# Kernel tuning notes

Hardware: AMD Instinct MI355X
Metric: run time of the kernel (lower is better)

Reference implementation:

```python
import jax, jax.numpy as jnp
import numpy as np

B, L, V, H = 2, 2048, 1024, 16
HD = V // H  # head size 64
EPS = 1e-3   # keras LayerNormalization default


def setup_inputs() -> dict:
    key = jax.random.key(0)
    ks = jax.random.split(key, 10)
    scale = 1.0 / np.sqrt(V)
    return {
        "query": jax.random.normal(ks[0], (B, L, V), jnp.float32),
        "key_t": jax.random.normal(ks[1], (B, L, V), jnp.float32),
        "value": jax.random.normal(ks[2], (B, L, V), jnp.float32),
        "Wq": jax.random.normal(ks[3], (H, V, HD), jnp.float32) * scale,
        "Wk": jax.random.normal(ks[4], (H, V, HD), jnp.float32) * scale,
        "Wv": jax.random.normal(ks[5], (H, V, HD), jnp.float32) * scale,
        "gamma": jnp.ones((V,), jnp.float32),
        "beta": jnp.zeros((V,), jnp.float32),
        "query_mask": jax.random.randint(ks[6], (B, L), 0, 2, jnp.int32),
        "value_mask": jax.random.randint(ks[7], (B, L), 0, 2, jnp.int32),
    }


def reference(query, key_t, value, Wq, Wk, Wv, gamma, beta, query_mask, value_mask):
    qm = query_mask.astype(jnp.float32)  # (B,L)
    vm = value_mask.astype(jnp.float32)  # (B,L)

    # per-head no-bias Dense projections, batched over heads
    Q = jnp.einsum('blv,hvd->bhld', query, Wq)
    K = jnp.einsum('blv,hvd->bhld', key_t, Wk)
    Vh = jnp.einsum('blv,hvd->bhld', value, Wv)

    scores = jnp.einsum('bhld,bhmd->bhlm', Q, K) / jnp.sqrt(jnp.float32(HD))
    attn = jax.nn.softmax(scores, axis=-1)

    # post-softmax multiplicative masking (faithful to original)
    tri = jnp.tril(jnp.ones((L, L), jnp.float32))  # (L,L) causal
    attn = attn * tri[None, None, :, :]
    attn = attn * qm[:, None, :, None] * vm[:, None, None, :]

    heads = jnp.einsum('bhlm,bhmd->bhld', attn, Vh)
    x = heads.transpose(0, 2, 1, 3).reshape(B, L, V)  # concat heads

    # dropout is identity at inference
    y = x + query
    mu = jnp.mean(y, axis=-1, keepdims=True)
    var = jnp.mean((y - mu) ** 2, axis=-1, keepdims=True)
    return gamma * (y - mu) * jax.lax.rsqrt(var + EPS) + beta
```

## Files before the change

kernel.cpp:

```cpp
#include <hip/hip_runtime.h>
#include <math.h>

constexpr int NB = 2;
constexpr int SL = 2048;
constexpr int NV = 1024;
constexpr int NH = 16;
constexpr int DH = 64;
constexpr int NT = SL / 64;
constexpr float LN_EPS = 1e-3f;

typedef __bf16 bf16_t;
typedef __bf16 v8bf __attribute__((ext_vector_type(8)));
typedef float  v4f  __attribute__((ext_vector_type(4)));

__device__ __forceinline__ v8bf cvt8(float4 a, float4 b) {
  v8bf v;
  v[0] = (bf16_t)a.x; v[1] = (bf16_t)a.y; v[2] = (bf16_t)a.z; v[3] = (bf16_t)a.w;
  v[4] = (bf16_t)b.x; v[5] = (bf16_t)b.y; v[6] = (bf16_t)b.z; v[7] = (bf16_t)b.w;
  return v;
}
__device__ __forceinline__ unsigned pack_bf16(float a, float b) {
  unsigned short ua = __builtin_bit_cast(unsigned short, (bf16_t)a);
  unsigned short ub = __builtin_bit_cast(unsigned short, (bf16_t)b);
  return (unsigned)ua | ((unsigned)ub << 16);
}
__device__ __forceinline__ void async_cp16(const void* g, void* l) {
  __builtin_amdgcn_global_load_lds(
      (const __attribute__((address_space(1))) unsigned int*)g,
      (__attribute__((address_space(3))) unsigned int*)l, 16, 0, 0);
}

__global__ __launch_bounds__(256)
void wcvt(const float* __restrict__ Wq, const float* __restrict__ Wk,
          const float* __restrict__ Wv, bf16_t* __restrict__ Wt) {
  __shared__ float ls[64][65];
  const int z = blockIdx.z;
  const float* W = z == 0 ? Wq : (z == 1 ? Wk : Wv);
  const float sc = z == 0 ? 0.125f * 1.44269504f : 1.0f;
  const int h = blockIdx.y, v0 = blockIdx.x * 64;
  const int t = threadIdx.x;
  const int rr = t >> 4, c4 = t & 15;
  const float* src = W + ((size_t)h * NV + v0) * DH;
#pragma unroll
  for (int it = 0; it < 4; ++it) {
    float4 f = *(const float4*)(src + (size_t)(rr + it * 16) * DH + c4 * 4);
    ls[rr + it * 16][c4 * 4 + 0] = f.x;
    ls[rr + it * 16][c4 * 4 + 1] = f.y;
    ls[rr + it * 16][c4 * 4 + 2] = f.z;
    ls[rr + it * 16][c4 * 4 + 3] = f.w;
  }
  __syncthreads();
  const int dd = t >> 2, vq = t & 3;
  bf16_t tmp[16];
#pragma unroll
  for (int i = 0; i < 16; ++i) tmp[i] = (bf16_t)(ls[vq * 16 + i][dd] * sc);
  bf16_t* dst = Wt + ((size_t)z * NV + h * 64 + dd) * NV + v0 + vq * 16;
  *(v8bf*)dst = *(v8bf*)&tmp[0];
  *(v8bf*)(dst + 8) = *(v8bf*)&tmp[8];
}

__global__ __launch_bounds__(256, 3)
void proj_mfma(const float* __restrict__ A0, const float* __restrict__ A1,
               const float* __restrict__ A2, const bf16_t* __restrict__ Wtb,
               const int* __restrict__ vmask,
               bf16_t* __restrict__ O0, bf16_t* __restrict__ O1,
               bf16_t* __restrict__ O2) {
  __shared__ __align__(16) float  As[2][128 * 32];
  __shared__ __align__(16) bf16_t Wsh[2][128 * 32];

  const int z = blockIdx.z;
  const float*  A   = z == 0 ? A0 : (z == 1 ? A1 : A2);
  bf16_t*       out = z == 0 ? O0 : (z == 1 ? O1 : O2);
  const bf16_t* W   = Wtb + (size_t)z * NV * NV;

  const int t = threadIdx.x, w = t >> 6, lane = t & 63;
  const int g = lane >> 4, lx = lane & 15;
  const int m0 = blockIdx.x * 128, n0 = blockIdx.y * 128;
  const int rbase = (w >> 1) * 64, cbase = (w & 1) * 64;

  auto stageA = [&](int k0, int buf) {
#pragma unroll
    for (int s = 0; s < 4; ++s) {
      const int r = w * 32 + s * 8 + (lane >> 3);
      const int c = (lane & 7) ^ (r & 7);
      async_cp16(A + (size_t)(m0 + r) * NV + k0 + c * 4,
                 (char*)As[buf] + (w * 32 + s * 8) * 128);
    }
  };
  auto stageW = [&](int k0, int buf) {
#pragma unroll
    for (int s = 0; s < 2; ++s) {
      const int r = w * 32 + s * 16 + (lane >> 2);
      const int c = (lane & 3) ^ (r & 3);
      async_cp16(W + (size_t)(n0 + r) * NV + k0 + c * 8,
                 (char*)Wsh[buf] + (w * 32 + s * 16) * 64);
    }
  };

  v4f acc[4][4] = {};
  stageA(0, 0);
  stageW(0, 0);

  for (int k0 = 0; k0 < NV; k0 += 32) {
    const int buf = (k0 >> 5) & 1;
    __syncthreads();
    if (k0 + 32 < NV) { stageA(k0 + 32, buf ^ 1); stageW(k0 + 32, buf ^ 1); }
    v8bf af[4], wf[4];
#pragma unroll
    for (int rt = 0; rt < 4; ++rt) {
      const int row = rbase + rt * 16 + lx;
      const int sw = row & 7;
      float4 f0 = *(const float4*)((const char*)As[buf] + row * 128 + ((2 * g)     ^ sw) * 16);
      float4 f1 = *(const float4*)((const char*)As[buf] + row * 128 + ((2 * g + 1) ^ sw) * 16);
      af[rt] = cvt8(f0, f1);
    }
#pragma unroll
    for (int ct = 0; ct < 4; ++ct) {
      const int row = cbase + ct * 16 + lx;
      wf[ct] = *(const v8bf*)((const char*)Wsh[buf] + row * 64 + (g ^ (row & 3)) * 16);
    }
#pragma unroll
    for (int rt = 0; rt < 4; ++rt)
#pragma unroll
      for (int ct = 0; ct < 4; ++ct)
        acc[rt][ct] = __builtin_amdgcn_mfma_f32_16x16x32_bf16(
            af[rt], wf[ct], acc[rt][ct], 0, 0, 0);
  }

  if (z < 2) {
#pragma unroll
    for (int rt = 0; rt < 4; ++rt) {
#pragma unroll
      for (int reg = 0; reg < 4; ++reg) {
        const int row = m0 + rbase + rt * 16 + g * 4 + reg;
        const int b = row >> 11, l = row & (SL - 1);
#pragma unroll
        for (int ct = 0; ct < 4; ++ct) {
          const int n = n0 + cbase + ct * 16 + lx;
          const int h = n >> 6, d = n & 63;
          out[((size_t)(b * NH + h) * SL + l) * DH + d] = (bf16_t)acc[rt][ct][reg];
        }
      }
    }
  } else {
#pragma unroll
    for (int rt = 0; rt < 4; ++rt) {
      const int row = m0 + rbase + rt * 16 + g * 4;
      const int b = row >> 11, l = row & (SL - 1);
      float vm0 = (float)vmask[b * SL + l + 0];
      float vm1 = (float)vmask[b * SL + l + 1];
      float vm2 = (float)vmask[b * SL + l + 2];
      float vm3 = (float)vmask[b * SL + l + 3];
#pragma unroll
      for (int ct = 0; ct < 4; ++ct) {
        const int n = n0 + cbase + ct * 16 + lx;
        const int h = n >> 6, d = n & 63;
        uint2 u = {pack_bf16(acc[rt][ct][0] * vm0, acc[rt][ct][1] * vm1),
                   pack_bf16(acc[rt][ct][2] * vm2, acc[rt][ct][3] * vm3)};
        *(uint2*)&out[((size_t)(b * NH + h) * DH + d) * SL + l] = u;
      }
    }
  }
}

__global__ __launch_bounds__(256, 3)
void attn_mfma(const bf16_t* __restrict__ Qg, const bf16_t* __restrict__ Kg,
               const bf16_t* __restrict__ Vtg_all, const int* __restrict__ qmask,
               float* __restrict__ Xout) {
  struct LoopBufs { bf16_t kbuf[2][64 * 64]; bf16_t vbuf[2][64 * 64]; };
  union __align__(16) SU { LoopBufs lp; float Obuf[2][64][36]; };
  __shared__ SU su;
  __shared__ bf16_t Ps[64][72];
  __shared__ float sums[2][64];

  const int id = blockIdx.x;
  const int bh = (id & 7) | ((id >> 8) << 3);
  const int qb = 31 - ((id >> 3) & 31);
  const int t = threadIdx.x, w = t >> 6, lane = t & 63;
  const int g = lane >> 4, lx = lane & 15;
  const int mh = w >> 1, qh = w & 1;
  const int b = bh >> 4, h = bh & 15;
  const int l0 = qb * 64;

  const bf16_t* Kb  = Kg + (size_t)bh * SL * DH;
  const bf16_t* Vtg = Vtg_all + (size_t)bh * DH * SL;

  v8bf qf[2][2];
#pragma unroll
  for (int qt = 0; qt < 2; ++qt)
#pragma unroll
    for (int ks = 0; ks < 2; ++ks)
      qf[qt][ks] = *(const v8bf*)&Qg[((size_t)bh * SL + l0 + qh * 32 + qt * 16 + lx) * DH +
                                     ks * 32 + g * 8];

  v4f O[2][4] = {};
  float suml[2] = {0.f, 0.f};

  auto stageK = [&](int mb, int buf) {
#pragma unroll
    for (int s = 0; s < 2; ++s) {
      const int r = w * 16 + s * 8 + (lane >> 3);
      const int c = (lane & 7) ^ (r & 7);
      async_cp16(Kb + (size_t)(mb + r) * DH + c * 8,
                 (char*)su.lp.kbuf[buf] + (w * 16 + s * 8) * 128);
    }
  };
  auto stageV = [&](int mb, int buf) {
#pragma unroll
    for (int s = 0; s < 2; ++s) {
      const int r = w * 16 + s * 8 + (lane >> 3);
      const int c = (lane & 7) ^ (r & 7);
      async_cp16(Vtg + (size_t)r * SL + mb + c * 8,
                 (char*)su.lp.vbuf[buf] + (w * 16 + s * 8) * 128);
    }
  };

  stageK(0, 0);
  stageV(0, 0);

  for (int mt = 0; mt <= qb; ++mt) {
    const int m0 = mt * 64, pb = mt & 1;
    __syncthreads();
    if (mt + 1 < NT)  stageK(m0 + 64, pb ^ 1);
    if (mt + 1 <= qb) stageV(m0 + 64, pb ^ 1);

    v4f S[2][2] = {};
#pragma unroll
    for (int ks = 0; ks < 2; ++ks)
#pragma unroll
      for (int mt2 = 0; mt2 < 2; ++mt2) {
        const int row = mh * 32 + mt2 * 16 + lx;
        const int slot = (ks * 4 + g) ^ (row & 7);
        v8bf kf = *(const v8bf*)((const char*)su.lp.kbuf[pb] + row * 128 + slot * 16);
#pragma unroll
        for (int qt = 0; qt < 2; ++qt)
          S[mt2][qt] = __builtin_amdgcn_mfma_f32_16x16x32_bf16(
              kf, qf[qt][ks], S[mt2][qt], 0, 0, 0);
      }

    const bool diag = (mt == qb);
#pragma unroll
    for (int mt2 = 0; mt2 < 2; ++mt2)
#pragma unroll
      for (int qt = 0; qt < 2; ++qt) {
        float e0 = __builtin_amdgcn_exp2f(S[mt2][qt][0]);
        float e1 = __builtin_amdgcn_exp2f(S[mt2][qt][1]);
        float e2 = __builtin_amdgcn_exp2f(S[mt2][qt][2]);
        float e3 = __builtin_amdgcn_exp2f(S[mt2][qt][3]);
        suml[qt] += (e0 + e1) + (e2 + e3);
        if (diag) {
          const int ml = mh * 32 + mt2 * 16 + g * 4;
          const int ql = qh * 32 + qt * 16 + lx;
          e0 = (ml + 0 <= ql) ? e0 : 0.f;
          e1 = (ml + 1 <= ql) ? e1 : 0.f;
          e2 = (ml + 2 <= ql) ? e2 : 0.f;
          e3 = (ml + 3 <= ql) ? e3 : 0.f;
        }
        uint2 u = {pack_bf16(e0, e1), pack_bf16(e2, e3)};
        *(uint2*)&Ps[qh * 32 + qt * 16 + lx][mh * 32 + mt2 * 16 + g * 4] = u;
      }

    v8bf pf[2];
#pragma unroll
    for (int qt = 0; qt < 2; ++qt)
      pf[qt] = *(const v8bf*)&Ps[qh * 32 + qt * 16 + lx][mh * 32 + g * 8];
#pragma unroll
    for (int dt = 0; dt < 4; ++dt) {
      const int row = dt * 16 + lx;
      const int slot = (mh * 4 + g) ^ (row & 7);
      v8bf vf = *(const v8bf*)((const char*)su.lp.vbuf[pb] + row * 128 + slot * 16);
#pragma unroll
      for (int qt = 0; qt < 2; ++qt)
        O[qt][dt] = __builtin_amdgcn_mfma_f32_16x16x32_bf16(
            pf[qt], vf, O[qt][dt], 0, 0, 0);
    }
  }

  for (int mt = qb + 1; mt < NT; ++mt) {
    const int pb = mt & 1;
    __syncthreads();
    if (mt + 1 < NT) stageK(mt * 64 + 64, pb ^ 1);
    v4f S[2][2] = {};
#pragma unroll
    for (int ks = 0; ks < 2; ++ks)
#pragma unroll
      for (int mt2 = 0; mt2 < 2; ++mt2) {
        const int row = mh * 32 + mt2 * 16 + lx;
        const int slot = (ks * 4 + g) ^ (row & 7);
        v8bf kf = *(const v8bf*)((const char*)su.lp.kbuf[pb] + row * 128 + slot * 16);
#pragma unroll
        for (int qt = 0; qt < 2; ++qt)
          S[mt2][qt] = __builtin_amdgcn_mfma_f32_16x16x32_bf16(
              kf, qf[qt][ks], S[mt2][qt], 0, 0, 0);
      }
#pragma unroll
    for (int mt2 = 0; mt2 < 2; ++mt2)
#pragma unroll
      for (int qt = 0; qt < 2; ++qt)
        suml[qt] += (__builtin_amdgcn_exp2f(S[mt2][qt][0]) +
                     __builtin_amdgcn_exp2f(S[mt2][qt][1])) +
                    (__builtin_amdgcn_exp2f(S[mt2][qt][2]) +
                     __builtin_amdgcn_exp2f(S[mt2][qt][3]));
  }

  suml[0] += __shfl_xor(suml[0], 16); suml[0] += __shfl_xor(suml[0], 32);
  suml[1] += __shfl_xor(suml[1], 16); suml[1] += __shfl_xor(suml[1], 32);
  __syncthreads();
  if (g == 0) {
    sums[mh][qh * 32 + lx]      = suml[0];
    sums[mh][qh * 32 + 16 + lx] = suml[1];
  }
  if (mh == 0) {
#pragma unroll
    for (int qt = 0; qt < 2; ++qt)
#pragma unroll
      for (int dt = 0; dt < 4; ++dt)
        *(v4f*)&su.Obuf[qh][dt * 16 + lx][qt * 16 + g * 4] = O[qt][dt];
  }
  __syncthreads();
  if (mh == 1) {
#pragma unroll
    for (int qt = 0; qt < 2; ++qt) {
#pragma unroll
      for (int dt = 0; dt < 4; ++dt)
        O[qt][dt] += *(const v4f*)&su.Obuf[qh][dt * 16 + lx][qt * 16 + g * 4];
#pragma unroll
      for (int reg = 0; reg < 4; ++reg) {
        const int ql = qh * 32 + qt * 16 + g * 4 + reg;
        const int q = l0 + ql;
        const float den = sums[0][ql] + sums[1][ql];
        const float inv = (float)qmask[b * SL + q] / den;
#pragma unroll
        for (int dt = 0; dt < 4; ++dt)
          Xout[((size_t)(b * SL + q)) * NV + h * DH + dt * 16 + lx] =
              O[qt][dt][reg] * inv;
      }
    }
  }
}

__global__ __launch_bounds__(256)
void ln_kernel(const float* __restrict__ X, const float* __restrict__ query,
               const float* __restrict__ gamma, const float* __restrict__ beta,
               float* __restrict__ out) {
  const int row0 = blockIdx.x * 2;
  const int t = threadIdx.x;
  float4 gv = *(const float4*)(gamma + t * 4);
  float4 bv = *(const float4*)(beta + t * 4);
  float y[2][4];
  float s[2], ss[2];
#pragma unroll
  for (int r = 0; r < 2; ++r) {
    float4 xv = *(const float4*)(X + (size_t)(row0 + r) * NV + t * 4);
    float4 qv = *(const float4*)(query + (size_t)(row0 + r) * NV + t * 4);
    y[r][0] = xv.x + qv.x; y[r][1] = xv.y + qv.y;
    y[r][2] = xv.z + qv.z; y[r][3] = xv.w + qv.w;
    s[r]  = (y[r][0] + y[r][1]) + (y[r][2] + y[r][3]);
    ss[r] = (y[r][0]*y[r][0] + y[r][1]*y[r][1]) + (y[r][2]*y[r][2] + y[r][3]*y[r][3]);
  }
#pragma unroll
  for (int off = 1; off < 64; off <<= 1) {
    s[0]  += __shfl_xor(s[0], off);  ss[0] += __shfl_xor(ss[0], off);
    s[1]  += __shfl_xor(s[1], off);  ss[1] += __shfl_xor(ss[1], off);
  }
  __shared__ float wsum[2][2][4];
  const int wid = t >> 6;
  if ((t & 63) == 0) {
    wsum[0][0][wid] = s[0]; wsum[0][1][wid] = ss[0];
    wsum[1][0][wid] = s[1]; wsum[1][1][wid] = ss[1];
  }
  __syncthreads();
#pragma unroll
  for (int r = 0; r < 2; ++r) {
    float sr  = (wsum[r][0][0] + wsum[r][0][1]) + (wsum[r][0][2] + wsum[r][0][3]);
    float ssr = (wsum[r][1][0] + wsum[r][1][1]) + (wsum[r][1][2] + wsum[r][1][3]);
    const float mu   = sr * (1.f / NV);
    const float var  = ssr * (1.f / NV) - mu * mu;
    const float rstd = rsqrtf(var + LN_EPS);
    float4 o;
    o.x = gv.x * (y[r][0] - mu) * rstd + bv.x;
    o.y = gv.y * (y[r][1] - mu) * rstd + bv.y;
    o.z = gv.z * (y[r][2] - mu) * rstd + bv.z;
    o.w = gv.w * (y[r][3] - mu) * rstd + bv.w;
    *(float4*)(out + (size_t)(row0 + r) * NV + t * 4) = o;
  }
}

extern "C" void kernel_launch(void* const* d_in, const int* in_sizes, int n_in,
                              void* d_out, int out_size, void* d_ws, size_t ws_size,
                              hipStream_t stream) {
  const float* query = (const float*)d_in[0];
  const float* key_t = (const float*)d_in[1];
  const float* value = (const float*)d_in[2];
  const float* Wq    = (const float*)d_in[3];
  const float* Wk    = (const float*)d_in[4];
  const float* Wv    = (const float*)d_in[5];
  const float* gamma = (const float*)d_in[6];
  const float* beta  = (const float*)d_in[7];
  const int*   qmask = (const int*)d_in[8];
  const int*   vmask = (const int*)d_in[9];
  float* out = (float*)d_out;

  const size_t per = (size_t)NB * NH * SL * DH;
  bf16_t* Qws = (bf16_t*)d_ws;
  bf16_t* Kws = Qws + per;
  bf16_t* Vws = Kws + per;
  bf16_t* Wtb = Vws + per;

  wcvt<<<dim3(16, 16, 3), 256, 0, stream>>>(Wq, Wk, Wv, Wtb);
  proj_mfma<<<dim3(32, 8, 3), 256, 0, stream>>>(query, key_t, value, Wtb,
                                                vmask, Qws, Kws, Vws);
  attn_mfma<<<1024, 256, 0, stream>>>(Qws, Kws, Vws, qmask, out);
  ln_kernel<<<NB * SL / 2, 256, 0, stream>>>(out, query, gamma, beta, out);
}
```

Measured before the change: 226.8 us.

## Enlarge attention query tile and convert projection A tiles to bf16 in registers

The attention kernel now gives each block 128 query rows, with each wave owning 32 queries across all 64 keys of a tile. This drops the cross-wave O and sum reduction through shared memory and halves the number of K/V tile loads per query. The projection kernel now loads fp32 activations into registers, converts them to bf16, and writes bf16 to padded LDS instead of staging fp32 with async copies, which halves LDS footprint and read traffic. In exchange the grid shrinks to 512 attention blocks, giving less parallelism and worse causal load balance, and the synchronous global loads for A may expose latency.

Measured after the change: 226.8 us. No clear change (-0.0%).

```diff
diff --git a/kernel.cpp b/kernel.cpp
--- a/kernel.cpp
+++ b/kernel.cpp
@@ -6,19 +6,12 @@
 constexpr int NV = 1024;
 constexpr int NH = 16;
 constexpr int DH = 64;
-constexpr int NT = SL / 64;
 constexpr float LN_EPS = 1e-3f;
 
 typedef __bf16 bf16_t;
 typedef __bf16 v8bf __attribute__((ext_vector_type(8)));
 typedef float  v4f  __attribute__((ext_vector_type(4)));
 
-__device__ __forceinline__ v8bf cvt8(float4 a, float4 b) {
-  v8bf v;
-  v[0] = (bf16_t)a.x; v[1] = (bf16_t)a.y; v[2] = (bf16_t)a.z; v[3] = (bf16_t)a.w;
-  v[4] = (bf16_t)b.x; v[5] = (bf16_t)b.y; v[6] = (bf16_t)b.z; v[7] = (bf16_t)b.w;
-  return v;
-}
 __device__ __forceinline__ unsigned pack_bf16(float a, float b) {
   unsigned short ua = __builtin_bit_cast(unsigned short, (bf16_t)a);
   unsigned short ub = __builtin_bit_cast(unsigned short, (bf16_t)b);
@@ -65,27 +58,37 @@
                const int* __restrict__ vmask,
                bf16_t* __restrict__ O0, bf16_t* __restrict__ O1,
                bf16_t* __restrict__ O2) {
-  __shared__ __align__(16) float  As[2][128 * 32];
-  __shared__ __align__(16) bf16_t Wsh[2][128 * 32];
-
-  const int z = blockIdx.z;
+  __shared__ __align__(16) bf16_t Asb[2][128 * 40];
+  __shared__ __align__(16) bf16_t Wsb[2][128 * 32];
+
+  const int id = blockIdx.x;
+  const int z = id >> 8;
+  const int m0 = (id & 31) * 128;
+  const int n0 = ((id >> 5) & 7) * 128;
   const float*  A   = z == 0 ? A0 : (z == 1 ? A1 : A2);
   bf16_t*       out = z == 0 ? O0 : (z == 1 ? O1 : O2);
   const bf16_t* W   = Wtb + (size_t)z * NV * NV;
 
   const int t = threadIdx.x, w = t >> 6, lane = t & 63;
   const int g = lane >> 4, lx = lane & 15;
-  const int m0 = blockIdx.x * 128, n0 = blockIdx.y * 128;
   const int rbase = (w >> 1) * 64, cbase = (w & 1) * 64;
 
-  auto stageA = [&](int k0, int buf) {
-#pragma unroll
-    for (int s = 0; s < 4; ++s) {
-      const int r = w * 32 + s * 8 + (lane >> 3);
-      const int c = (lane & 7) ^ (r & 7);
-      async_cp16(A + (size_t)(m0 + r) * NV + k0 + c * 4,
-                 (char*)As[buf] + (w * 32 + s * 8) * 128);
-    }
+  const int ar_r = t >> 1;
+  const int ar_h = (t & 1) * 16;
+  float4 ar[4];
+  auto gloadA = [&](int k0) {
+#pragma unroll
+    for (int s = 0; s < 4; ++s)
+      ar[s] = *(const float4*)(A + (size_t)(m0 + ar_r) * NV + k0 + ar_h + s * 4);
+  };
+  auto writeA = [&](int buf) {
+    const int c0 = (ar_h >> 3);
+    uint4 u0 = {pack_bf16(ar[0].x, ar[0].y), pack_bf16(ar[0].z, ar[0].w),
+                pack_bf16(ar[1].x, ar[1].y), pack_bf16(ar[1].z, ar[1].w)};
+    uint4 u1 = {pack_bf16(ar[2].x, ar[2].y), pack_bf16(ar[2].z, ar[2].w),
+                pack_bf16(ar[3].x, ar[3].y), pack_bf16(ar[3].z, ar[3].w)};
+    *(uint4*)((char*)Asb[buf] + ar_r * 80 + (c0 + 0) * 16) = u0;
+    *(uint4*)((char*)Asb[buf] + ar_r * 80 + (c0 + 1) * 16) = u1;
   };
   auto stageW = [&](int k0, int buf) {
 #pragma unroll
@@ -93,31 +96,31 @@
       const int r = w * 32 + s * 16 + (lane >> 2);
       const int c = (lane & 3) ^ (r & 3);
       async_cp16(W + (size_t)(n0 + r) * NV + k0 + c * 8,
-                 (char*)Wsh[buf] + (w * 32 + s * 16) * 64);
+                 (char*)Wsb[buf] + (w * 32 + s * 16) * 64);
     }
   };
 
   v4f acc[4][4] = {};
-  stageA(0, 0);
+
+  gloadA(0);
   stageW(0, 0);
-
-  for (int k0 = 0; k0 < NV; k0 += 32) {
-    const int buf = (k0 >> 5) & 1;
-    __syncthreads();
-    if (k0 + 32 < NV) { stageA(k0 + 32, buf ^ 1); stageW(k0 + 32, buf ^ 1); }
+  writeA(0);
+  __syncthreads();
+
+  for (int it = 0; it < 32; ++it) {
+    const int buf = it & 1;
+    if (it < 31) { gloadA((it + 1) * 32); stageW((it + 1) * 32, buf ^ 1); }
     v8bf af[4], wf[4];
 #pragma unroll
     for (int rt = 0; rt < 4; ++rt) {
       const int row = rbase + rt * 16 + lx;
-      const int sw = row & 7;
-      float4 f0 = *(const float4*)((const char*)As[buf] + row * 128 + ((2 * g)     ^ sw) * 16);
-      float4 f1 = *(const float4*)((const char*)As[buf] + row * 128 + ((2 * g + 1) ^ sw) * 16);
-      af[rt] = cvt8(f0, f1);
+      af[rt] = *(const v8bf*)((const char*)Asb[buf] + row * 80 + g * 16);
     }
 #pragma unroll
     for (int ct = 0; ct < 4; ++ct) {
       const int row = cbase + ct * 16 + lx;
-      wf[ct] = *(const v8bf*)((const char*)Wsh[buf] + row * 64 + (g ^ (row & 3)) * 16);
+      wf[ct] = *(const v8bf*)((const char*)Wsb[buf] + row * 64 +
+                              ((g ^ (row & 3)) * 16));
     }
 #pragma unroll
     for (int rt = 0; rt < 4; ++rt)
@@ -125,6 +128,7 @@
       for (int ct = 0; ct < 4; ++ct)
         acc[rt][ct] = __builtin_amdgcn_mfma_f32_16x16x32_bf16(
             af[rt], wf[ct], acc[rt][ct], 0, 0, 0);
+    if (it < 31) { writeA(buf ^ 1); __syncthreads(); }
   }
 
   if (z < 2) {
@@ -167,20 +171,18 @@
 void attn_mfma(const bf16_t* __restrict__ Qg, const bf16_t* __restrict__ Kg,
                const bf16_t* __restrict__ Vtg_all, const int* __restrict__ qmask,
                float* __restrict__ Xout) {
-  struct LoopBufs { bf16_t kbuf[2][64 * 64]; bf16_t vbuf[2][64 * 64]; };
-  union __align__(16) SU { LoopBufs lp; float Obuf[2][64][36]; };
-  __shared__ SU su;
-  __shared__ bf16_t Ps[64][72];
-  __shared__ float sums[2][64];
+  __shared__ __align__(16) bf16_t kbuf[2][64 * 64];
+  __shared__ __align__(16) bf16_t vbuf[2][64 * 64];
+  __shared__ __align__(16) bf16_t Ps[4][32][72];
 
   const int id = blockIdx.x;
-  const int bh = (id & 7) | ((id >> 8) << 3);
-  const int qb = 31 - ((id >> 3) & 31);
+  const int bh = (id & 7) | ((id >> 7) << 3);
+  const int qb = 15 - ((id >> 3) & 15);
   const int t = threadIdx.x, w = t >> 6, lane = t & 63;
   const int g = lane >> 4, lx = lane & 15;
-  const int mh = w >> 1, qh = w & 1;
   const int b = bh >> 4, h = bh & 15;
-  const int l0 = qb * 64;
+  const int l0 = qb * 128;
+  const int lastAct = 2 * qb + 1;
 
   const bf16_t* Kb  = Kg + (size_t)bh * SL * DH;
   const bf16_t* Vtg = Vtg_all + (size_t)bh * DH * SL;
@@ -190,57 +192,63 @@
   for (int qt = 0; qt < 2; ++qt)
 #pragma unroll
     for (int ks = 0; ks < 2; ++ks)
-      qf[qt][ks] = *(const v8bf*)&Qg[((size_t)bh * SL + l0 + qh * 32 + qt * 16 + lx) * DH +
+      qf[qt][ks] = *(const v8bf*)&Qg[((size_t)bh * SL + l0 + w * 32 + qt * 16 + lx) * DH +
                                      ks * 32 + g * 8];
 
   v4f O[2][4] = {};
   float suml[2] = {0.f, 0.f};
 
+  const int sr_off = lane >> 3, sc_l = lane & 7;
   auto stageK = [&](int mb, int buf) {
 #pragma unroll
     for (int s = 0; s < 2; ++s) {
-      const int r = w * 16 + s * 8 + (lane >> 3);
-      const int c = (lane & 7) ^ (r & 7);
+      const int r = w * 16 + s * 8 + sr_off;
+      const int c = sc_l ^ (r & 7);
       async_cp16(Kb + (size_t)(mb + r) * DH + c * 8,
-                 (char*)su.lp.kbuf[buf] + (w * 16 + s * 8) * 128);
+                 (char*)kbuf[buf] + (w * 16 + s * 8) * 128);
     }
   };
   auto stageV = [&](int mb, int buf) {
 #pragma unroll
     for (int s = 0; s < 2; ++s) {
-      const int r = w * 16 + s * 8 + (lane >> 3);
-      const int c = (lane & 7) ^ (r & 7);
+      const int r = w * 16 + s * 8 + sr_off;
+      const int c = sc_l ^ (r & 7);
       async_cp16(Vtg + (size_t)r * SL + mb + c * 8,
-                 (char*)su.lp.vbuf[buf] + (w * 16 + s * 8) * 128);
+                 (char*)vbuf[buf] + (w * 16 + s * 8) * 128);
     }
   };
 
   stageK(0, 0);
   stageV(0, 0);
 
-  for (int mt = 0; mt <= qb; ++mt) {
-    const int m0 = mt * 64, pb = mt & 1;
+  for (int mt = 0; mt <= lastAct; ++mt) {
+    const int pb = mt & 1;
     __syncthreads();
-    if (mt + 1 < NT)  stageK(m0 + 64, pb ^ 1);
-    if (mt + 1 <= qb) stageV(m0 + 64, pb ^ 1);
-
-    v4f S[2][2] = {};
+    if (mt < SL / 64 - 1)  stageK((mt + 1) * 64, pb ^ 1);
+    if (mt + 1 <= lastAct) stageV((mt + 1) * 64, pb ^ 1);
+
+    v4f S[4][2];
+#pragma unroll
+    for (int mt2 = 0; mt2 < 4; ++mt2) {
+      S[mt2][0] = (v4f){0.f, 0.f, 0.f, 0.f};
+      S[mt2][1] = (v4f){0.f, 0.f, 0.f, 0.f};
+    }
 #pragma unroll
     for (int ks = 0; ks < 2; ++ks)
 #pragma unroll
-      for (int mt2 = 0; mt2 < 2; ++mt2) {
-        const int row = mh * 32 + mt2 * 16 + lx;
-        const int slot = (ks * 4 + g) ^ (row & 7);
-        v8bf kf = *(const v8bf*)((const char*)su.lp.kbuf[pb] + row * 128 + slot * 16);
+      for (int mt2 = 0; mt2 < 4; ++mt2) {
+        const int row = mt2 * 16 + lx;
+        v8bf kf = *(const v8bf*)((const char*)kbuf[pb] + row * 128 +
+                                 (((ks * 4 + g) ^ (lx & 7)) * 16));
 #pragma unroll
         for (int qt = 0; qt < 2; ++qt)
           S[mt2][qt] = __builtin_amdgcn_mfma_f32_16x16x32_bf16(
               kf, qf[qt][ks], S[mt2][qt], 0, 0, 0);
       }
 
-    const bool diag = (mt == qb);
-#pragma unroll
-    for (int mt2 = 0; mt2 < 2; ++mt2)
+    const bool diagzone = (mt >= 2 * qb);
+#pragma unroll
+    for (int mt2 = 0; mt2 < 4; ++mt2)
 #pragma unroll
       for (int qt = 0; qt < 2; ++qt) {
         float e0 = __builtin_amdgcn_exp2f(S[mt2][qt][0]);
@@ -248,53 +256,61 @@
         float e2 = __builtin_amdgcn_exp2f(S[mt2][qt][2]);
         float e3 = __builtin_amdgcn_exp2f(S[mt2][qt][3]);
         suml[qt] += (e0 + e1) + (e2 + e3);
-        if (diag) {
-          const int ml = mh * 32 + mt2 * 16 + g * 4;
-          const int ql = qh * 32 + qt * 16 + lx;
+        if (diagzone) {
+          const int ml = mt * 64 + mt2 * 16 + g * 4;
+          const int ql = l0 + w * 32 + qt * 16 + lx;
           e0 = (ml + 0 <= ql) ? e0 : 0.f;
           e1 = (ml + 1 <= ql) ? e1 : 0.f;
           e2 = (ml + 2 <= ql) ? e2 : 0.f;
           e3 = (ml + 3 <= ql) ? e3 : 0.f;
         }
         uint2 u = {pack_bf16(e0, e1), pack_bf16(e2, e3)};
-        *(uint2*)&Ps[qh * 32 + qt * 16 + lx][mh * 32 + mt2 * 16 + g * 4] = u;
-      }
-
-    v8bf pf[2];
-#pragma unroll
-    for (int qt = 0; qt < 2; ++qt)
-      pf[qt] = *(const v8bf*)&Ps[qh * 32 + qt * 16 + lx][mh * 32 + g * 8];
-#pragma unroll
-    for (int dt = 0; dt < 4; ++dt) {
-      const int row = dt * 16 + lx;
-      const int slot = (mh * 4 + g) ^ (row & 7);
-      v8bf vf = *(const v8bf*)((const char*)su.lp.vbuf[pb] + row * 128 + slot * 16);
+        *(uint2*)&Ps[w][qt * 16 + lx][mt2 * 16 + g * 4] = u;
+      }
+
+#pragma unroll
+    for (int ks = 0; ks < 2; ++ks) {
+      v8bf pf[2];
 #pragma unroll
       for (int qt = 0; qt < 2; ++qt)
-        O[qt][dt] = __builtin_amdgcn_mfma_f32_16x16x32_bf16(
-            pf[qt], vf, O[qt][dt], 0, 0, 0);
-    }
-  }
-
-  for (int mt = qb + 1; mt < NT; ++mt) {
+        pf[qt] = *(const v8bf*)&Ps[w][qt * 16 + lx][ks * 32 + g * 8];
+#pragma unroll
+      for (int dt = 0; dt < 4; ++dt) {
+        const int row = dt * 16 + lx;
+        v8bf vf = *(const v8bf*)((const char*)vbuf[pb] + row * 128 +
+                                 (((ks * 4 + g) ^ (lx & 7)) * 16));
+#pragma unroll
+        for (int qt = 0; qt < 2; ++qt)
+          O[qt][dt] = __builtin_amdgcn_mfma_f32_16x16x32_bf16(
+              pf[qt], vf, O[qt][dt], 0, 0, 0);
+      }
+    }
+  }
+
+  for (int mt = lastAct + 1; mt < SL / 64; ++mt) {
     const int pb = mt & 1;
     __syncthreads();
-    if (mt + 1 < NT) stageK(mt * 64 + 64, pb ^ 1);
-    v4f S[2][2] = {};
+    if (mt < SL / 64 - 1) stageK((mt + 1) * 64, pb ^ 1);
+    v4f S[4][2];
+#pragma unroll
+    for (int mt2 = 0; mt2 < 4; ++mt2) {
+      S[mt2][0] = (v4f){0.f, 0.f, 0.f, 0.f};
+      S[mt2][1] = (v4f){0.f, 0.f, 0.f, 0.f};
+    }
 #pragma unroll
     for (int ks = 0; ks < 2; ++ks)
 #pragma unroll
-      for (int mt2 = 0; mt2 < 2; ++mt2) {
-        const int row = mh * 32 + mt2 * 16 + lx;
-        const int slot = (ks * 4 + g) ^ (row & 7);
-        v8bf kf = *(const v8bf*)((const char*)su.lp.kbuf[pb] + row * 128 + slot * 16);
+      for (int mt2 = 0; mt2 < 4; ++mt2) {
+        const int row = mt2 * 16 + lx;
+        v8bf kf = *(const v8bf*)((const char*)kbuf[pb] + row * 128 +
+                                 (((ks * 4 + g) ^ (lx & 7)) * 16));
 #pragma unroll
         for (int qt = 0; qt < 2; ++qt)
           S[mt2][qt] = __builtin_amdgcn_mfma_f32_16x16x32_bf16(
               kf, qf[qt][ks], S[mt2][qt], 0, 0, 0);
       }
 #pragma unroll
-    for (int mt2 = 0; mt2 < 2; ++mt2)
+    for (int mt2 = 0; mt2 < 4; ++mt2)
 #pragma unroll
       for (int qt = 0; qt < 2; ++qt)
         suml[qt] += (__builtin_amdgcn_exp2f(S[mt2][qt][0]) +
@@ -305,36 +321,17 @@
 
   suml[0] += __shfl_xor(suml[0], 16); suml[0] += __shfl_xor(suml[0], 32);
   suml[1] += __shfl_xor(suml[1], 16); suml[1] += __shfl_xor(suml[1], 32);
-  __syncthreads();
-  if (g == 0) {
-    sums[mh][qh * 32 + lx]      = suml[0];
-    sums[mh][qh * 32 + 16 + lx] = suml[1];
-  }
-  if (mh == 0) {
-#pragma unroll
-    for (int qt = 0; qt < 2; ++qt)
+#pragma unroll
+  for (int qt = 0; qt < 2; ++qt) {
+#pragma unroll
+    for (int reg = 0; reg < 4; ++reg) {
+      const int q = l0 + w * 32 + qt * 16 + g * 4 + reg;
+      const float den = __shfl(suml[qt], g * 4 + reg);
+      const float inv = (float)qmask[b * SL + q] / den;
 #pragma unroll
       for (int dt = 0; dt < 4; ++dt)
-        *(v4f*)&su.Obuf[qh][dt * 16 + lx][qt * 16 + g * 4] = O[qt][dt];
-  }
-  __syncthreads();
-  if (mh == 1) {
-#pragma unroll
-    for (int qt = 0; qt < 2; ++qt) {
-#pragma unroll
-      for (int dt = 0; dt < 4; ++dt)
-        O[qt][dt] += *(const v4f*)&su.Obuf[qh][dt * 16 + lx][qt * 16 + g * 4];
-#pragma unroll
-      for (int reg = 0; reg < 4; ++reg) {
-        const int ql = qh * 32 + qt * 16 + g * 4 + reg;
-        const int q = l0 + ql;
-        const float den = sums[0][ql] + sums[1][ql];
-        const float inv = (float)qmask[b * SL + q] / den;
-#pragma unroll
-        for (int dt = 0; dt < 4; ++dt)
-          Xout[((size_t)(b * SL + q)) * NV + h * DH + dt * 16 + lx] =
-              O[qt][dt][reg] * inv;
-      }
+        Xout[((size_t)(b * SL + q)) * NV + h * DH + dt * 16 + lx] =
+            O[qt][dt][reg] * inv;
     }
   }
 }
@@ -408,8 +405,8 @@
   bf16_t* Wtb = Vws + per;
 
   wcvt<<<dim3(16, 16, 3), 256, 0, stream>>>(Wq, Wk, Wv, Wtb);
-  proj_mfma<<<dim3(32, 8, 3), 256, 0, stream>>>(query, key_t, value, Wtb,
-                                                vmask, Qws, Kws, Vws);
-  attn_mfma<<<1024, 256, 0, stream>>>(Qws, Kws, Vws, qmask, out);
+  proj_mfma<<<768, 256, 0, stream>>>(query, key_t, value, Wtb,
+                                     vmask, Qws, Kws, Vws);
+  attn_mfma<<<512, 256, 0, stream>>>(Qws, Kws, Vws, qmask, out);
   ln_kernel<<<NB * SL / 2, 256, 0, stream>>>(out, query, gamma, beta, out);
 }
```
